# Optimization experiments

Hardware: AMD Instinct MI355X
Metric: run time of the kernel (lower is better)

Reference implementation:

```python
import jax, jax.numpy as jnp
import numpy as np

H, DH = 16, 64  # heads, dim_head (inner_dim = 1024)
VARIANCE_CONSTANT = 1.0


def setup_inputs() -> dict:
    key = jax.random.key(0)
    ks = jax.random.split(key, 6)
    b, n, m, dim = 8, 4096, 64, 1024
    inner = H * DH
    x = jax.random.normal(ks[0], (b, n, dim), dtype=jnp.float32)
    latents = jax.random.normal(ks[1], (b, m, dim), dtype=jnp.float32)
    mask = jax.random.randint(ks[2], (b, n), 0, 2).astype(bool)  # True = masked out
    sd = 1.0 / np.sqrt(dim)
    Wq = jax.random.normal(ks[3], (inner, dim), dtype=jnp.float32) * sd
    Wkv = jax.random.normal(ks[4], (2 * inner, dim), dtype=jnp.float32) * sd
    Wout = jax.random.normal(ks[5], (dim, inner), dtype=jnp.float32) * sd
    return {"x": x, "latents": latents, "mask": mask, "Wq": Wq, "Wkv": Wkv, "Wout": Wout}


def _split_heads(t):  # b n (h d) -> b h n d
    b, n, _ = t.shape
    return t.reshape(b, n, H, DH).transpose(0, 2, 1, 3)


def reference(x, latents, mask, Wq, Wkv, Wout):
    b, n, dim = x.shape
    scale = DH ** -0.5
    q = latents @ Wq.T                      # b m inner
    k, v = jnp.split(x @ Wkv.T, 2, axis=-1)  # b n inner each
    q = _split_heads(q) * scale             # b h m d
    k = _split_heads(k)                     # b h n d
    v = _split_heads(v)
    sim = jnp.einsum('bhid,bhjd->bhij', q, k)  # b h m n
    max_neg = -jnp.finfo(sim.dtype).max
    sim = jnp.where(mask[:, None, None, :], max_neg, sim)
    sim_new = sim - jax.lax.stop_gradient(sim.max(axis=-1, keepdims=True))
    # cross-query (dim=-2) unbiased variance -> std over latents, shape b h n
    std = jnp.sqrt(jnp.var(sim_new, axis=-2, ddof=1) + 1e-4)
    std = jnp.where(mask[:, None, :], VARIANCE_CONSTANT, std)
    loss_variance = jnp.mean(jax.nn.relu(VARIANCE_CONSTANT - std))
    attn = jax.nn.softmax(sim_new, axis=-1)
    out = jnp.einsum('bhij,bhjd->bhid', attn, v)         # b h m d
    out = out.transpose(0, 2, 1, 3).reshape(b, -1, H * DH)  # b m inner
    out = out @ Wout.T                                    # b m dim
    return out, loss_variance
```

## Files before the change

### kernel.cpp

```cpp
#include <hip/hip_runtime.h>


using u16 = unsigned short;
typedef short bf16x8_t __attribute__((ext_vector_type(8)));
typedef float f32x4_t __attribute__((ext_vector_type(4)));

__device__ __forceinline__ u16 f2bf(float f) {
    union { float f; unsigned u; } v; v.f = f;
    unsigned r = v.u + 0x7fffu + ((v.u >> 16) & 1u);
    return (u16)(r >> 16);
}

template <typename T> __device__ __forceinline__ T cvt_out(float v);
template <> __device__ __forceinline__ float cvt_out<float>(float v) { return v; }
template <> __device__ __forceinline__ u16   cvt_out<u16>(float v)   { return f2bf(v); }

__device__ __forceinline__ void cp16(const void* g, void* l) {
    __builtin_amdgcn_global_load_lds((const __attribute__((address_space(1))) unsigned int*)g,
                                     (__attribute__((address_space(3))) unsigned int*)l, 16, 0, 0);
}

__global__ void cvt_all(const float* __restrict__ x, const float* __restrict__ lat,
                        const float* __restrict__ wq, const float* __restrict__ wkv,
                        const float* __restrict__ wout,
                        u16* __restrict__ xb, u16* __restrict__ latb,
                        u16* __restrict__ wqb, u16* __restrict__ wkvb,
                        u16* __restrict__ woutb) {
    int i = blockIdx.x * 256 + threadIdx.x;
    const float* s; u16* d; int off; float sc = 1.f;
    if (i < 8388608)      { s = x;    d = xb;    off = i; }
    else if (i < 8519680) { s = lat;  d = latb;  off = i - 8388608; }
    else if (i < 8781824) { s = wq;   d = wqb;   off = i - 8519680; sc = 0.125f; }
    else if (i < 9306112) { s = wkv;  d = wkvb;  off = i - 8781824; }
    else if (i < 9568256) { s = wout; d = woutb; off = i - 9306112; }
    else return;
    float4 v = ((const float4*)s)[off];
    ushort4 o;
    o.x = f2bf(v.x * sc); o.y = f2bf(v.y * sc);
    o.z = f2bf(v.z * sc); o.w = f2bf(v.w * sc);
    ((ushort4*)d)[off] = o;
}


__device__ __forceinline__ void stage_half(const u16* __restrict__ G, u16* L,
                                           int grow0, int kt, int tid) {
    const int row8 = tid >> 3;
    const int pcb = tid & 7;
    const int sc = (pcb ^ (row8 & 7)) * 8;
    const int k0 = kt * 64;
    const int wu = (tid >> 6) * 512;
#pragma unroll
    for (int r = 0; r < 2; ++r)
        cp16(G + (size_t)(grow0 + r * 64 + row8) * 1024 + k0 + sc, L + r * 4096 + wu);
}

template <bool E12, bool E34, int WAIT>
__device__ __forceinline__ void tile_phases(
    const u16* At, const u16* Bt,
    const u16* __restrict__ gA, u16* lA, int rowA, int ktA,
    const u16* __restrict__ gB, u16* lB, int rowB, int ktB,
    int wm, int wn, int frow, int pc0, int pc1, int tid,
    f32x4_t (&acc)[8][4]) {
    bf16x8_t aF[4][2], bF[4][2];
#pragma unroll
    for (int i = 0; i < 4; ++i) {
        const u16* p = At + (wm * 128 + i * 16 + frow) * 64;
        aF[i][0] = *(const bf16x8_t*)(p + pc0);
        aF[i][1] = *(const bf16x8_t*)(p + pc1);
    }
#pragma unroll
    for (int j = 0; j < 4; ++j)
        bF[j][0] = *(const bf16x8_t*)(Bt + (wn * 64 + j * 16 + frow) * 64 + pc0);
    if (E12) stage_half(gA, lA, rowA, ktA, tid);
    __builtin_amdgcn_s_barrier();
    asm volatile("s_waitcnt lgkmcnt(0)" ::: "memory");
    __builtin_amdgcn_s_setprio(1);
#pragma unroll
    for (int i = 0; i < 4; ++i)
#pragma unroll
        for (int j = 0; j < 4; ++j)
            acc[i][j] = __builtin_amdgcn_mfma_f32_16x16x32_bf16(aF[i][0], bF[j][0], acc[i][j], 0, 0, 0);
    __builtin_amdgcn_s_setprio(0);
    __builtin_amdgcn_s_barrier();
#pragma unroll
    for (int j = 0; j < 4; ++j)
        bF[j][1] = *(const bf16x8_t*)(Bt + (wn * 64 + j * 16 + frow) * 64 + pc1);
    if (E12) stage_half(gA, lA + 8192, rowA + 128, ktA, tid);
    __builtin_amdgcn_s_barrier();
    asm volatile("s_waitcnt lgkmcnt(0)" ::: "memory");
    __builtin_amdgcn_s_setprio(1);
#pragma unroll
    for (int i = 0; i < 4; ++i)
#pragma unroll
        for (int j = 0; j < 4; ++j)
            acc[i][j] = __builtin_amdgcn_mfma_f32_16x16x32_bf16(aF[i][1], bF[j][1], acc[i][j], 0, 0, 0);
    __builtin_amdgcn_s_setprio(0);
    __builtin_amdgcn_s_barrier();
#pragma unroll
    for (int i = 0; i < 4; ++i) {
        const u16* p = At + (wm * 128 + (i + 4) * 16 + frow) * 64;
        aF[i][0] = *(const bf16x8_t*)(p + pc0);
        aF[i][1] = *(const bf16x8_t*)(p + pc1);
    }
    if (E34) stage_half(gB, lB, rowB, ktB, tid);
    __builtin_amdgcn_s_barrier();
    asm volatile("s_waitcnt lgkmcnt(0)" ::: "memory");
    __builtin_amdgcn_s_setprio(1);
#pragma unroll
    for (int i = 0; i < 4; ++i)
#pragma unroll
        for (int j = 0; j < 4; ++j)
            acc[i + 4][j] = __builtin_amdgcn_mfma_f32_16x16x32_bf16(aF[i][0], bF[j][0], acc[i + 4][j], 0, 0, 0);
    __builtin_amdgcn_s_setprio(0);
    __builtin_amdgcn_s_barrier();
    if (E34) stage_half(gB, lB + 8192, rowB + 128, ktB, tid);
    if (WAIT == 4)      asm volatile("s_waitcnt vmcnt(4)" ::: "memory");
    else if (WAIT == 0) asm volatile("s_waitcnt vmcnt(0)" ::: "memory");
    __builtin_amdgcn_s_barrier();
    __builtin_amdgcn_s_setprio(1);
#pragma unroll
    for (int i = 0; i < 4; ++i)
#pragma unroll
        for (int j = 0; j < 4; ++j)
            acc[i + 4][j] = __builtin_amdgcn_mfma_f32_16x16x32_bf16(aF[i][1], bF[j][1], acc[i + 4][j], 0, 0, 0);
    __builtin_amdgcn_s_setprio(0);
    __builtin_amdgcn_s_barrier();
}

__global__ __launch_bounds__(512, 2) void gemm_kv8(const u16* __restrict__ A,
                                                   const u16* __restrict__ B,
                                                   const u16* __restrict__ Qb,
                                                   const int* __restrict__ mask,
                                                   u16* __restrict__ Kc,
                                                   u16* __restrict__ Vt,
                                                   float* __restrict__ Mg2) {
    __shared__ __align__(16) u16 smem[65536];
    u16* A0 = smem;
    u16* A1 = smem + 16384;
    u16* B0 = smem + 32768;
    u16* B1 = smem + 49152;
    const int tid = threadIdx.x;
    const int wid = tid >> 6, lane = tid & 63;
    const int wm = wid >> 2, wn = wid & 3;
    const int frow = lane & 15, fq = lane >> 4;
    const int pc0 = (fq ^ (frow & 7)) * 8;
    const int pc1 = ((4 + fq) ^ (frow & 7)) * 8;
    const int fid = blockIdx.x;
    const int xcd = fid & 7, l = fid >> 3;
    const int by = xcd * 16 + (l >> 3), bx = l & 7;
    const int bm = by * 256, bn = bx * 256;

    f32x4_t acc[8][4];
#pragma unroll
    for (int i = 0; i < 8; ++i)
#pragma unroll
        for (int j = 0; j < 4; ++j) acc[i][j] = (f32x4_t){0.f, 0.f, 0.f, 0.f};

    stage_half(B, B0, bn, 0, tid);        stage_half(B, B0 + 8192, bn + 128, 0, tid);
    stage_half(A, A0, bm, 0, tid);        stage_half(A, A0 + 8192, bm + 128, 0, tid);
    stage_half(B, B1, bn, 1, tid);        stage_half(B, B1 + 8192, bn + 128, 1, tid);
    asm volatile("s_waitcnt vmcnt(4)" ::: "memory");
    __builtin_amdgcn_s_barrier();

    for (int t = 0; t < 7; ++t) {
        tile_phases<true, true, 4>(A0, B0, A, A1, bm, 2 * t + 1, B, B0, bn, 2 * t + 2,
                                   wm, wn, frow, pc0, pc1, tid, acc);
        tile_phases<true, true, 4>(A1, B1, A, A0, bm, 2 * t + 2, B, B1, bn, 2 * t + 3,
                                   wm, wn, frow, pc0, pc1, tid, acc);
    }
    tile_phases<true, false, 0>(A0, B0, A, A1, bm, 15, B, B1, bn, 0,
                                wm, wn, frow, pc0, pc1, tid, acc);
    tile_phases<false, false, -1>(A1, B1, A, A0, bm, 0, B, B1, bn, 0,
                                  wm, wn, frow, pc0, pc1, tid, acc);

    if (bx < 4) {
        const int bb = bm >> 12, jb = bm & 4095, chunk = by & 15;
        u16* Kl = smem;
#pragma unroll
        for (int i = 0; i < 8; ++i)
#pragma unroll
            for (int j = 0; j < 4; ++j) {
                const int cc0 = wn * 64 + j * 16 + frow;
#pragma unroll
                for (int r = 0; r < 4; ++r) {
                    const int jr = wm * 128 + i * 16 + fq * 4 + r;
                    Kl[jr * 256 + (((cc0 >> 3) ^ (jr & 7)) * 8) + (cc0 & 7)] = f2bf(acc[i][j][r]);
                }
            }
        __syncthreads();
#pragma unroll
        for (int p = 0; p < 16; ++p) {
            const int idx = p * 512 + tid;
            const int jr = idx >> 5, cb = idx & 31;
            bf16x8_t v = *(const bf16x8_t*)(Kl + jr * 256 + ((cb ^ (jr & 7)) * 8));
            *(bf16x8_t*)(Kc + (size_t)(bm + jr) * 1024 + bn + cb * 8) = v;
        }
        const int hh = wid >> 1, jn = (wid & 1) * 128;
        const int hc = (bx << 2) + hh;
        int mk[8];
#pragma unroll
        for (int jf = 0; jf < 8; ++jf)
            mk[jf] = mask[bb * 4096 + jb + jn + jf * 16 + frow];
        f32x4_t s2[4][8];
#pragma unroll
        for (int i = 0; i < 4; ++i)
#pragma unroll
            for (int jf = 0; jf < 8; ++jf) s2[i][jf] = (f32x4_t){0.f, 0.f, 0.f, 0.f};
#pragma unroll
        for (int ks = 0; ks < 2; ++ks) {
            bf16x8_t aq[4], bk[8];
#pragma unroll
            for (int i = 0; i < 4; ++i)
                aq[i] = *(const bf16x8_t*)(Qb + (size_t)(bb * 64 + i * 16 + frow) * 1024 +
                                           hc * 64 + ks * 32 + fq * 8);
#pragma unroll
            for (int jf = 0; jf < 8; ++jf) {
                const int jr = jn + jf * 16 + frow;
                bk[jf] = *(const bf16x8_t*)(Kl + jr * 256 +
                                            (((hh * 8 + ks * 4 + fq) ^ (jr & 7)) * 8));
            }
#pragma unroll
            for (int i = 0; i < 4; ++i)
#pragma unroll
                for (int jf = 0; jf < 8; ++jf)
                    s2[i][jf] = __builtin_amdgcn_mfma_f32_16x16x32_bf16(aq[i], bk[jf], s2[i][jf], 0, 0, 0);
        }
        float ml[16];
#pragma unroll
        for (int i = 0; i < 16; ++i) ml[i] = -3.0e38f;
#pragma unroll
        for (int jf = 0; jf < 8; ++jf)
            if (!mk[jf])
#pragma unroll
                for (int i = 0; i < 4; ++i)
#pragma unroll
                    for (int r = 0; r < 4; ++r)
                        ml[i * 4 + r] = fmaxf(ml[i * 4 + r], s2[i][jf][r]);
#pragma unroll
        for (int i = 0; i < 16; ++i) {
            float v = ml[i];
            v = fmaxf(v, __shfl_xor(v, 1)); v = fmaxf(v, __shfl_xor(v, 2));
            v = fmaxf(v, __shfl_xor(v, 4)); v = fmaxf(v, __shfl_xor(v, 8));
            ml[i] = v;
        }
        __syncthreads();
        float* Mp = (float*)smem;
        if ((lane & 15) == 0)
#pragma unroll
            for (int i = 0; i < 4; ++i)
#pragma unroll
                for (int r = 0; r < 4; ++r)
                    Mp[wid * 64 + i * 16 + fq * 4 + r] = ml[i * 4 + r];
        __syncthreads();
        if (tid < 256) {
            const int h2 = tid >> 6, m = tid & 63;
            Mg2[((size_t)(bb * 16 + (bx << 2) + h2) * 16 + chunk) * 64 + m] =
                fmaxf(Mp[(2 * h2) * 64 + m], Mp[(2 * h2 + 1) * 64 + m]);
        }
        return;
    }

    const int vb0 = bn - 1024;
    const int b = bm >> 12, jb = bm & 4095;
    u16* Ct = smem;
#pragma unroll
    for (int ph = 0; ph < 2; ++ph) {
        __syncthreads();
        if ((wn >> 1) == ph) {
#pragma unroll
            for (int i = 0; i < 8; ++i)
#pragma unroll
                for (int j = 0; j < 4; ++j) {
                    const int vdl = (wn & 1) * 64 + j * 16 + frow;
                    const int jl = wm * 128 + i * 16 + fq * 4;
                    ushort4 pk;
                    pk.x = f2bf(acc[i][j][0]); pk.y = f2bf(acc[i][j][1]);
                    pk.z = f2bf(acc[i][j][2]); pk.w = f2bf(acc[i][j][3]);
                    *(ushort4*)(Ct + vdl * 264 + jl) = pk;
                }
        }
        __syncthreads();
#pragma unroll
        for (int p = 0; p < 8; ++p) {
            const int idx = p * 512 + tid;
            const int vdl = idx >> 5;
            const int jl = (idx & 31) * 8;
            bf16x8_t v = *(const bf16x8_t*)(Ct + vdl * 264 + jl);
            const int vd = vb0 + ph * 128 + vdl;
            const size_t addr = ((size_t)(b * 16 + (vd >> 6)) * 64 + (vd & 63)) * 4096 + jb + jl;
            *(bf16x8_t*)(Vt + addr) = v;
        }
    }
}

template <typename OutT>
__global__ __launch_bounds__(256) void gemm_bt64(const u16* __restrict__ A,
                                                 const u16* __restrict__ B,
                                                 OutT* __restrict__ C,
                                                 int M, int N, int K) {
    __shared__ __align__(16) u16 As[64 * 64];
    __shared__ __align__(16) u16 Bs[64 * 64];
    const int tid = threadIdx.x;
    const int wid = tid >> 6, lane = tid & 63;
    const int bm = blockIdx.y * 64, bn = blockIdx.x * 64;
    const int srow = lane >> 3;
    const int scol = ((lane & 7) ^ srow) * 8;
    const int frow = lane & 15;
    const int wr = (wid >> 1) * 32, wc = (wid & 1) * 32;

    f32x4_t acc[2][2];
#pragma unroll
    for (int i = 0; i < 2; ++i)
#pragma unroll
        for (int j = 0; j < 2; ++j) acc[i][j] = (f32x4_t){0.f, 0.f, 0.f, 0.f};

    for (int k0 = 0; k0 < K; k0 += 64) {
#pragma unroll
        for (int t = 0; t < 2; ++t) {
            const int c = wid * 2 + t;
            const int r = c * 8 + srow;
            cp16(A + (size_t)(bm + r) * K + k0 + scol, As + c * 512);
            cp16(B + (size_t)(bn + r) * K + k0 + scol, Bs + c * 512);
        }
        __syncthreads();
#pragma unroll
        for (int ks = 0; ks < 2; ++ks) {
            const int grp = (((ks * 4 + (lane >> 4)) ^ (frow & 7)) * 8);
            bf16x8_t af[2], bfv[2];
#pragma unroll
            for (int i = 0; i < 2; ++i) {
                af[i]  = *(const bf16x8_t*)(As + (wr + i * 16 + frow) * 64 + grp);
                bfv[i] = *(const bf16x8_t*)(Bs + (wc + i * 16 + frow) * 64 + grp);
            }
#pragma unroll
            for (int i = 0; i < 2; ++i)
#pragma unroll
                for (int j = 0; j < 2; ++j)
                    acc[i][j] = __builtin_amdgcn_mfma_f32_16x16x32_bf16(af[i], bfv[j], acc[i][j], 0, 0, 0);
        }
        __syncthreads();
    }
    const int cr = (lane >> 4) * 4, cc = lane & 15;
#pragma unroll
    for (int i = 0; i < 2; ++i)
#pragma unroll
        for (int j = 0; j < 2; ++j) {
            size_t base = (size_t)(bm + wr + i * 16 + cr) * N + (bn + wc + j * 16 + cc);
#pragma unroll
            for (int r = 0; r < 4; ++r)
                C[base + (size_t)r * N] = cvt_out<OutT>(acc[i][j][r]);
        }
}

__global__ __launch_bounds__(256, 2) void attn_pv(const u16* __restrict__ q,
                                                  const u16* __restrict__ kbuf,
                                                  const u16* __restrict__ vtbuf,
                                                  const int* __restrict__ mask,
                                                  const float* __restrict__ Mg,
                                                  float* __restrict__ Opart,
                                                  float* __restrict__ Rpart,
                                                  float* __restrict__ loss) {
    const int c = blockIdx.x & 3, bh = blockIdx.x >> 2, b = bh >> 4, h = bh & 15;
    const int tid = threadIdx.x, wid = tid >> 6, lane = tid & 63;
    const int frow = lane & 15, cr = (lane >> 4) * 4;
    const int srow = lane >> 3, scol = ((lane & 7) ^ srow) * 8;

    __shared__ __align__(16) u16 qs[64 * 64];
    __shared__ __align__(16) u16 wbuf[4][2][4096];
    __shared__ float Mrow[64];
    __shared__ float RpS[4][64];
    __shared__ float lossP[4];

    const size_t kbase  = (size_t)b * 4096 * 1024 + (size_t)h * 64;
    const size_t vtbase = (size_t)bh * 64 * 4096;
    const int cb = c * 1024;
    u16* Kw = &wbuf[wid][0][0];
    u16* Vw = &wbuf[wid][1][0];

#pragma unroll
    for (int t = 0; t < 2; ++t) {
        int cq = wid * 2 + t;
        int r = cq * 8 + srow;
        cp16(q + (size_t)(b * 64 + r) * 1024 + h * 64 + scol, qs + cq * 512);
    }
    if (tid < 64) {
        float m = -3.0e38f;
#pragma unroll
        for (int cc = 0; cc < 16; ++cc) m = fmaxf(m, Mg[(size_t)(bh * 16 + cc) * 64 + tid]);
        Mrow[tid] = m;
    }
    __syncthreads();

    f32x4_t oacc[4][4];
#pragma unroll
    for (int i = 0; i < 4; ++i)
#pragma unroll
        for (int j = 0; j < 4; ++j) oacc[i][j] = (f32x4_t){0.f, 0.f, 0.f, 0.f};
    float rloc[16];
#pragma unroll
    for (int i = 0; i < 16; ++i) rloc[i] = 0.f;
    float lossacc = 0.f;

    for (int sc = 0; sc < 4; ++sc) {
        const int j0 = cb + (sc * 4 + wid) * 64;
#pragma unroll
        for (int t = 0; t < 8; ++t) {
            int r = t * 8 + srow;
            cp16(kbuf + kbase + (size_t)(j0 + r) * 1024 + scol, Kw + t * 512);
        }
#pragma unroll
        for (int t = 0; t < 8; ++t) {
            int d = t * 8 + srow;
            cp16(vtbuf + vtbase + (size_t)d * 4096 + j0 + scol, Vw + t * 512);
        }
        __builtin_amdgcn_s_waitcnt(0);

        f32x4_t sacc[4][4];
#pragma unroll
        for (int i = 0; i < 4; ++i)
#pragma unroll
            for (int j = 0; j < 4; ++j) sacc[i][j] = (f32x4_t){0.f, 0.f, 0.f, 0.f};
#pragma unroll
        for (int ks2 = 0; ks2 < 2; ++ks2) {
            const int grp = (((ks2 * 4 + (lane >> 4)) ^ (frow & 7)) * 8);
            bf16x8_t af[4], bfv[4];
#pragma unroll
            for (int i = 0; i < 4; ++i) {
                af[i]  = *(const bf16x8_t*)(qs + (i * 16 + frow) * 64 + grp);
                bfv[i] = *(const bf16x8_t*)(Kw + (i * 16 + frow) * 64 + grp);
            }
#pragma unroll
            for (int i = 0; i < 4; ++i)
#pragma unroll
                for (int j = 0; j < 4; ++j)
                    sacc[i][j] = __builtin_amdgcn_mfma_f32_16x16x32_bf16(af[i], bfv[j], sacc[i][j], 0, 0, 0);
        }

#pragma unroll
        for (int nt = 0; nt < 4; ++nt) {
            const int jl = nt * 16 + frow;
            const bool msk = mask[b * 4096 + j0 + jl] != 0;
            const int jh = jl >> 3, jlo = jl & 7;
            float c1 = 0.f, c2 = 0.f;
#pragma unroll
            for (int mt = 0; mt < 4; ++mt) {
#pragma unroll
                for (int r = 0; r < 4; ++r) {
                    const int row = mt * 16 + cr + r;
                    const float t = sacc[mt][nt][r] - Mrow[row];
                    const float p = msk ? 0.f : __expf(t);
                    rloc[mt * 4 + r] += p;
                    c1 += msk ? 0.f : t;
                    c2 += msk ? 0.f : t * t;
                    Kw[row * 64 + ((jh ^ (row & 7)) * 8) + jlo] = f2bf(p);
                }
            }
            c1 += __shfl_xor(c1, 16); c1 += __shfl_xor(c1, 32);
            c2 += __shfl_xor(c2, 16); c2 += __shfl_xor(c2, 32);
            if (lane < 16 && !msk) {
                const float var = (c2 - c1 * c1 * (1.f / 64.f)) * (1.f / 63.f);
                lossacc += fmaxf(1.f - sqrtf(var + 1e-4f), 0.f);
            }
        }
#pragma unroll
        for (int ks2 = 0; ks2 < 2; ++ks2) {
            const int grp = (((ks2 * 4 + (lane >> 4)) ^ (frow & 7)) * 8);
            bf16x8_t pa[4], vb[4];
#pragma unroll
            for (int i = 0; i < 4; ++i) {
                pa[i] = *(const bf16x8_t*)(Kw + (i * 16 + frow) * 64 + grp);
                vb[i] = *(const bf16x8_t*)(Vw + (i * 16 + frow) * 64 + grp);
            }
#pragma unroll
            for (int i = 0; i < 4; ++i)
#pragma unroll
                for (int j = 0; j < 4; ++j)
                    oacc[i][j] = __builtin_amdgcn_mfma_f32_16x16x32_bf16(pa[i], vb[j], oacc[i][j], 0, 0, 0);
        }
    }

    float* Osw = (float*)(&wbuf[0][0][0]) + wid * 4096;
#pragma unroll
    for (int i = 0; i < 4; ++i)
#pragma unroll
        for (int j = 0; j < 4; ++j)
#pragma unroll
            for (int r = 0; r < 4; ++r)
                Osw[(i * 16 + cr + r) * 64 + j * 16 + frow] = oacc[i][j][r];

#pragma unroll
    for (int i = 0; i < 16; ++i) {
        float v = rloc[i];
        v += __shfl_xor(v, 1); v += __shfl_xor(v, 2);
        v += __shfl_xor(v, 4); v += __shfl_xor(v, 8);
        rloc[i] = v;
    }
    if ((lane & 15) == 0) {
#pragma unroll
        for (int mt = 0; mt < 4; ++mt)
#pragma unroll
            for (int r = 0; r < 4; ++r)
                RpS[wid][mt * 16 + cr + r] = rloc[mt * 4 + r];
    }
    float v = lossacc;
    v += __shfl_xor(v, 1); v += __shfl_xor(v, 2); v += __shfl_xor(v, 4);
    v += __shfl_xor(v, 8); v += __shfl_xor(v, 16); v += __shfl_xor(v, 32);
    if (lane == 0) lossP[wid] = v;
    __syncthreads();

    const float4* Ob4 = (const float4*)(&wbuf[0][0][0]);
    const size_t ob = (size_t)(bh * 4 + c) * 4096;
#pragma unroll
    for (int p = 0; p < 4; ++p) {
        const int e = tid + p * 256;
        float4 s0 = Ob4[e];
        float4 s1 = Ob4[e + 1024];
        float4 s2 = Ob4[e + 2048];
        float4 s3 = Ob4[e + 3072];
        float4 o;
        o.x = s0.x + s1.x + s2.x + s3.x;
        o.y = s0.y + s1.y + s2.y + s3.y;
        o.z = s0.z + s1.z + s2.z + s3.z;
        o.w = s0.w + s1.w + s2.w + s3.w;
        ((float4*)(Opart + ob))[e] = o;
    }
    if (tid < 64)
        Rpart[(size_t)(bh * 4 + c) * 64 + tid] =
            RpS[0][tid] + RpS[1][tid] + RpS[2][tid] + RpS[3][tid];
    if (tid == 0)
        atomicAdd(loss, (lossP[0] + lossP[1] + lossP[2] + lossP[3]) * (1.f / 524288.f));
}

__global__ __launch_bounds__(256) void attn_fin(const float* __restrict__ Opart,
                                                const float* __restrict__ Rpart,
                                                u16* __restrict__ ao) {
    const int bh = blockIdx.x, b = bh >> 4, h = bh & 15;
    const int tid = threadIdx.x;
    __shared__ float Rt[64];
    if (tid < 64) {
        float r = 0.f;
#pragma unroll
        for (int cc = 0; cc < 4; ++cc) r += Rpart[(size_t)(bh * 4 + cc) * 64 + tid];
        Rt[tid] = r;
    }
    __syncthreads();
    for (int e = tid; e < 4096; e += 256) {
        float o = 0.f;
#pragma unroll
        for (int cc = 0; cc < 4; ++cc) o += Opart[(size_t)(bh * 4 + cc) * 4096 + e];
        const int row = e >> 6, d = e & 63;
        ao[(size_t)(b * 64 + row) * 1024 + h * 64 + d] = f2bf(o / Rt[row]);
    }
}

extern "C" void kernel_launch(void* const* d_in, const int* in_sizes, int n_in,
                              void* d_out, int out_size, void* d_ws, size_t ws_size,
                              hipStream_t stream) {
    const float* x    = (const float*)d_in[0];
    const float* lat  = (const float*)d_in[1];
    const int*   mask = (const int*)d_in[2];
    const float* Wq   = (const float*)d_in[3];
    const float* Wkv  = (const float*)d_in[4];
    const float* Wout = (const float*)d_in[5];
    float* out = (float*)d_out;

    char* ws = (char*)d_ws;
    u16* x_bf    = (u16*)(ws);
    u16* kbuf    = (u16*)(ws + 67108864);
    u16* vtbuf   = (u16*)(ws + 134217728);
    u16* wq_bf   = (u16*)(ws + 201326592);
    u16* wkv_bf  = (u16*)(ws + 203423744);
    u16* wout_bf = (u16*)(ws + 207618048);
    u16* lat_bf  = (u16*)(ws + 209715200);
    u16* q_bf    = (u16*)(ws + 210763776);
    u16* ao_bf   = (u16*)(ws + 211812352);
    float* Mg    = (float*)(ws + 201326592);
    float* Opart = (float*)(ws + 1048576);
    float* Rpart = (float*)(ws + 1048576 + 8388608);

    hipMemsetAsync(out + 524288, 0, 4, stream);

    cvt_all<<<37376, 256, 0, stream>>>(x, lat, Wq, Wkv, Wout,
                                       x_bf, lat_bf, wq_bf, wkv_bf, wout_bf);

    dim3 blk(256);
    gemm_bt64<u16><<<dim3(16, 8), blk, 0, stream>>>(lat_bf, wq_bf, q_bf, 512, 1024, 1024);
    gemm_kv8<<<dim3(1024), dim3(512), 0, stream>>>(x_bf, wkv_bf, q_bf, mask, kbuf, vtbuf, Mg);
    attn_pv<<<512, blk, 0, stream>>>(q_bf, kbuf, vtbuf, mask, Mg, Opart, Rpart, out + 524288);
    attn_fin<<<128, blk, 0, stream>>>(Opart, Rpart, ao_bf);
    gemm_bt64<float><<<dim3(16, 8), blk, 0, stream>>>(ao_bf, wout_bf, out, 512, 1024, 1024);
}
```

Measured before the change: 435.4 us.

## Split attn_pv waves by query rows with shared double-buffered K/V tiles

Reworks attn_pv so each wave owns 16 query rows across all keys instead of 64 rows over its own key slice. K/V tiles are shared by the block and double-buffered, with global-to-LDS prefetch of the next tile overlapping compute. Cross-query variance sums are reduced through LDS per tile, and the final cross-wave O reduction is dropped. Lower LDS and register use allows raising launch bounds to 3 blocks, at the cost of two to three block barriers per tile.

```diff
diff --git a/kernel.cpp b/kernel.cpp
--- a/kernel.cpp
+++ b/kernel.cpp
@@ -352,7 +352,7 @@
         }
 }
 
-__global__ __launch_bounds__(256, 2) void attn_pv(const u16* __restrict__ q,
+__global__ __launch_bounds__(256, 3) void attn_pv(const u16* __restrict__ q,
                                                   const u16* __restrict__ kbuf,
                                                   const u16* __restrict__ vtbuf,
                                                   const int* __restrict__ mask,
@@ -362,26 +362,26 @@
                                                   float* __restrict__ loss) {
     const int c = blockIdx.x & 3, bh = blockIdx.x >> 2, b = bh >> 4, h = bh & 15;
     const int tid = threadIdx.x, wid = tid >> 6, lane = tid & 63;
-    const int frow = lane & 15, cr = (lane >> 4) * 4;
-    const int srow = lane >> 3, scol = ((lane & 7) ^ srow) * 8;
-
-    __shared__ __align__(16) u16 qs[64 * 64];
-    __shared__ __align__(16) u16 wbuf[4][2][4096];
+    const int frow = lane & 15, fq = lane >> 4;
+    const int srow = lane >> 3, scol8 = ((lane & 7) ^ srow) * 8;
+
+    __shared__ __align__(16) u16 qs[4096];
+    __shared__ __align__(16) u16 kv[4][4096];
+    __shared__ __align__(16) u16 Pw[4][1024];
+    __shared__ float cstat[4][2][64];
     __shared__ float Mrow[64];
-    __shared__ float RpS[4][64];
-    __shared__ float lossP[4];
 
     const size_t kbase  = (size_t)b * 4096 * 1024 + (size_t)h * 64;
     const size_t vtbase = (size_t)bh * 64 * 4096;
     const int cb = c * 1024;
-    u16* Kw = &wbuf[wid][0][0];
-    u16* Vw = &wbuf[wid][1][0];
+    const int s_c = tid & 7, s_r0 = tid >> 3;
+    const int wu = wid * 512;
 
 #pragma unroll
     for (int t = 0; t < 2; ++t) {
         int cq = wid * 2 + t;
         int r = cq * 8 + srow;
-        cp16(q + (size_t)(b * 64 + r) * 1024 + h * 64 + scol, qs + cq * 512);
+        cp16(q + (size_t)(b * 64 + r) * 1024 + h * 64 + scol8, qs + cq * 512);
     }
     if (tid < 64) {
         float m = -3.0e38f;
@@ -389,146 +389,159 @@
         for (int cc = 0; cc < 16; ++cc) m = fmaxf(m, Mg[(size_t)(bh * 16 + cc) * 64 + tid]);
         Mrow[tid] = m;
     }
-    __syncthreads();
-
-    f32x4_t oacc[4][4];
-#pragma unroll
-    for (int i = 0; i < 4; ++i)
-#pragma unroll
-        for (int j = 0; j < 4; ++j) oacc[i][j] = (f32x4_t){0.f, 0.f, 0.f, 0.f};
-    float rloc[16];
-#pragma unroll
-    for (int i = 0; i < 16; ++i) rloc[i] = 0.f;
+#pragma unroll
+    for (int sel = 0; sel < 2; ++sel) {
+        const int j0 = cb + sel * 64;
+#pragma unroll
+        for (int rnd = 0; rnd < 2; ++rnd) {
+            const int row = rnd * 32 + s_r0;
+            const int sc = (s_c ^ (row & 7)) * 8;
+            cp16(kbuf + kbase + (size_t)(j0 + row) * 1024 + sc, kv[sel] + rnd * 2048 + wu);
+        }
+#pragma unroll
+        for (int rnd = 0; rnd < 2; ++rnd) {
+            const int row = rnd * 32 + s_r0;
+            const int sc = (s_c ^ (row & 7)) * 8;
+            cp16(vtbuf + vtbase + (size_t)row * 4096 + j0 + sc, kv[2 + sel] + rnd * 2048 + wu);
+        }
+    }
+    asm volatile("s_waitcnt vmcnt(4) lgkmcnt(0)" ::: "memory");
+    __builtin_amdgcn_s_barrier();
+
+    bf16x8_t af[2];
+#pragma unroll
+    for (int ks = 0; ks < 2; ++ks)
+        af[ks] = *(const bf16x8_t*)(qs + (wid * 16 + frow) * 64 + (((ks * 4 + fq) ^ (frow & 7)) * 8));
+    float mr[4];
+#pragma unroll
+    for (int r = 0; r < 4; ++r) mr[r] = Mrow[wid * 16 + fq * 4 + r];
+
+    f32x4_t oacc[4];
+#pragma unroll
+    for (int dj = 0; dj < 4; ++dj) oacc[dj] = (f32x4_t){0.f, 0.f, 0.f, 0.f};
+    float rloc[4] = {0.f, 0.f, 0.f, 0.f};
     float lossacc = 0.f;
 
-    for (int sc = 0; sc < 4; ++sc) {
-        const int j0 = cb + (sc * 4 + wid) * 64;
-#pragma unroll
-        for (int t = 0; t < 8; ++t) {
-            int r = t * 8 + srow;
-            cp16(kbuf + kbase + (size_t)(j0 + r) * 1024 + scol, Kw + t * 512);
-        }
-#pragma unroll
-        for (int t = 0; t < 8; ++t) {
-            int d = t * 8 + srow;
-            cp16(vtbuf + vtbase + (size_t)d * 4096 + j0 + scol, Vw + t * 512);
-        }
-        __builtin_amdgcn_s_waitcnt(0);
-
-        f32x4_t sacc[4][4];
-#pragma unroll
-        for (int i = 0; i < 4; ++i)
-#pragma unroll
-            for (int j = 0; j < 4; ++j) sacc[i][j] = (f32x4_t){0.f, 0.f, 0.f, 0.f};
-#pragma unroll
-        for (int ks2 = 0; ks2 < 2; ++ks2) {
-            const int grp = (((ks2 * 4 + (lane >> 4)) ^ (frow & 7)) * 8);
-            bf16x8_t af[4], bfv[4];
-#pragma unroll
-            for (int i = 0; i < 4; ++i) {
-                af[i]  = *(const bf16x8_t*)(qs + (i * 16 + frow) * 64 + grp);
-                bfv[i] = *(const bf16x8_t*)(Kw + (i * 16 + frow) * 64 + grp);
-            }
-#pragma unroll
-            for (int i = 0; i < 4; ++i)
-#pragma unroll
-                for (int j = 0; j < 4; ++j)
-                    sacc[i][j] = __builtin_amdgcn_mfma_f32_16x16x32_bf16(af[i], bfv[j], sacc[i][j], 0, 0, 0);
-        }
-
-#pragma unroll
-        for (int nt = 0; nt < 4; ++nt) {
-            const int jl = nt * 16 + frow;
-            const bool msk = mask[b * 4096 + j0 + jl] != 0;
-            const int jh = jl >> 3, jlo = jl & 7;
-            float c1 = 0.f, c2 = 0.f;
-#pragma unroll
-            for (int mt = 0; mt < 4; ++mt) {
-#pragma unroll
-                for (int r = 0; r < 4; ++r) {
-                    const int row = mt * 16 + cr + r;
-                    const float t = sacc[mt][nt][r] - Mrow[row];
-                    const float p = msk ? 0.f : __expf(t);
-                    rloc[mt * 4 + r] += p;
-                    c1 += msk ? 0.f : t;
-                    c2 += msk ? 0.f : t * t;
-                    Kw[row * 64 + ((jh ^ (row & 7)) * 8) + jlo] = f2bf(p);
-                }
-            }
-            c1 += __shfl_xor(c1, 16); c1 += __shfl_xor(c1, 32);
-            c2 += __shfl_xor(c2, 16); c2 += __shfl_xor(c2, 32);
-            if (lane < 16 && !msk) {
-                const float var = (c2 - c1 * c1 * (1.f / 64.f)) * (1.f / 63.f);
+    for (int t = 0; t < 16; ++t) {
+        const int sel = t & 1;
+        const int j0 = cb + t * 64;
+        const u16* Kc_ = kv[sel];
+        const u16* Vc_ = kv[2 + sel];
+        int mk[4];
+#pragma unroll
+        for (int j = 0; j < 4; ++j) mk[j] = mask[b * 4096 + j0 + j * 16 + frow];
+
+        f32x4_t sacc[4];
+#pragma unroll
+        for (int j = 0; j < 4; ++j) sacc[j] = (f32x4_t){0.f, 0.f, 0.f, 0.f};
+#pragma unroll
+        for (int ks = 0; ks < 2; ++ks) {
+            const int kswz = ((ks * 4 + fq) ^ (frow & 7)) * 8;
+#pragma unroll
+            for (int j = 0; j < 4; ++j) {
+                bf16x8_t bk = *(const bf16x8_t*)(Kc_ + (j * 16 + frow) * 64 + kswz);
+                sacc[j] = __builtin_amdgcn_mfma_f32_16x16x32_bf16(af[ks], bk, sacc[j], 0, 0, 0);
+            }
+        }
+        float c1l[4] = {0.f, 0.f, 0.f, 0.f}, c2l[4] = {0.f, 0.f, 0.f, 0.f};
+#pragma unroll
+        for (int j = 0; j < 4; ++j) {
+#pragma unroll
+            for (int r = 0; r < 4; ++r) {
+                const int rowl = fq * 4 + r;
+                const float tv = sacc[j][r] - mr[r];
+                const float p = mk[j] ? 0.f : __expf(tv);
+                rloc[r] += p;
+                c1l[j] += mk[j] ? 0.f : tv;
+                c2l[j] += mk[j] ? 0.f : tv * tv;
+                const int jc = j * 2 + (frow >> 3);
+                Pw[wid][rowl * 64 + ((jc ^ (rowl & 7)) * 8) + (frow & 7)] = f2bf(p);
+            }
+            c1l[j] += __shfl_xor(c1l[j], 16); c1l[j] += __shfl_xor(c1l[j], 32);
+            c2l[j] += __shfl_xor(c2l[j], 16); c2l[j] += __shfl_xor(c2l[j], 32);
+            if (fq == 0) {
+                cstat[wid][0][j * 16 + frow] = c1l[j];
+                cstat[wid][1][j * 16 + frow] = c2l[j];
+            }
+        }
+        asm volatile("s_waitcnt lgkmcnt(0)" ::: "memory");
+        __builtin_amdgcn_s_barrier();
+        if (wid == 0) {
+            const float c1t = cstat[0][0][lane] + cstat[1][0][lane] + cstat[2][0][lane] + cstat[3][0][lane];
+            const float c2t = cstat[0][1][lane] + cstat[1][1][lane] + cstat[2][1][lane] + cstat[3][1][lane];
+            if (!mask[b * 4096 + j0 + lane]) {
+                const float var = (c2t - c1t * c1t * (1.f / 64.f)) * (1.f / 63.f);
                 lossacc += fmaxf(1.f - sqrtf(var + 1e-4f), 0.f);
             }
         }
 #pragma unroll
-        for (int ks2 = 0; ks2 < 2; ++ks2) {
-            const int grp = (((ks2 * 4 + (lane >> 4)) ^ (frow & 7)) * 8);
-            bf16x8_t pa[4], vb[4];
-#pragma unroll
-            for (int i = 0; i < 4; ++i) {
-                pa[i] = *(const bf16x8_t*)(Kw + (i * 16 + frow) * 64 + grp);
-                vb[i] = *(const bf16x8_t*)(Vw + (i * 16 + frow) * 64 + grp);
-            }
-#pragma unroll
-            for (int i = 0; i < 4; ++i)
-#pragma unroll
-                for (int j = 0; j < 4; ++j)
-                    oacc[i][j] = __builtin_amdgcn_mfma_f32_16x16x32_bf16(pa[i], vb[j], oacc[i][j], 0, 0, 0);
-        }
-    }
-
-    float* Osw = (float*)(&wbuf[0][0][0]) + wid * 4096;
-#pragma unroll
-    for (int i = 0; i < 4; ++i)
-#pragma unroll
-        for (int j = 0; j < 4; ++j)
-#pragma unroll
-            for (int r = 0; r < 4; ++r)
-                Osw[(i * 16 + cr + r) * 64 + j * 16 + frow] = oacc[i][j][r];
-
-#pragma unroll
-    for (int i = 0; i < 16; ++i) {
-        float v = rloc[i];
+        for (int ks = 0; ks < 2; ++ks) {
+            const int kswz = ((ks * 4 + fq) ^ (frow & 7)) * 8;
+            bf16x8_t pa = *(const bf16x8_t*)(Pw[wid] + frow * 64 + kswz);
+#pragma unroll
+            for (int dj = 0; dj < 4; ++dj) {
+                bf16x8_t vb = *(const bf16x8_t*)(Vc_ + (dj * 16 + frow) * 64 + kswz);
+                oacc[dj] = __builtin_amdgcn_mfma_f32_16x16x32_bf16(pa, vb, oacc[dj], 0, 0, 0);
+            }
+        }
+        asm volatile("s_waitcnt lgkmcnt(0)" ::: "memory");
+        __builtin_amdgcn_s_barrier();
+        if (t < 14) {
+            const int jn = cb + (t + 2) * 64;
+#pragma unroll
+            for (int rnd = 0; rnd < 2; ++rnd) {
+                const int row = rnd * 32 + s_r0;
+                const int sc = (s_c ^ (row & 7)) * 8;
+                cp16(kbuf + kbase + (size_t)(jn + row) * 1024 + sc, kv[sel] + rnd * 2048 + wu);
+            }
+#pragma unroll
+            for (int rnd = 0; rnd < 2; ++rnd) {
+                const int row = rnd * 32 + s_r0;
+                const int sc = (s_c ^ (row & 7)) * 8;
+                cp16(vtbuf + vtbase + (size_t)row * 4096 + jn + sc, kv[2 + sel] + rnd * 2048 + wu);
+            }
+            asm volatile("s_waitcnt vmcnt(4)" ::: "memory");
+            __builtin_amdgcn_s_barrier();
+        } else if (t == 14) {
+            asm volatile("s_waitcnt vmcnt(0)" ::: "memory");
+            __builtin_amdgcn_s_barrier();
+        }
+    }
+
+    float* Ol = (float*)&kv[0][0];
+#pragma unroll
+    for (int dj = 0; dj < 4; ++dj)
+#pragma unroll
+        for (int r = 0; r < 4; ++r)
+            Ol[(wid * 16 + fq * 4 + r) * 64 + dj * 16 + frow] = oacc[dj][r];
+
+#pragma unroll
+    for (int r = 0; r < 4; ++r) {
+        float v = rloc[r];
         v += __shfl_xor(v, 1); v += __shfl_xor(v, 2);
         v += __shfl_xor(v, 4); v += __shfl_xor(v, 8);
-        rloc[i] = v;
-    }
-    if ((lane & 15) == 0) {
-#pragma unroll
-        for (int mt = 0; mt < 4; ++mt)
-#pragma unroll
-            for (int r = 0; r < 4; ++r)
-                RpS[wid][mt * 16 + cr + r] = rloc[mt * 4 + r];
-    }
-    float v = lossacc;
-    v += __shfl_xor(v, 1); v += __shfl_xor(v, 2); v += __shfl_xor(v, 4);
-    v += __shfl_xor(v, 8); v += __shfl_xor(v, 16); v += __shfl_xor(v, 32);
-    if (lane == 0) lossP[wid] = v;
-    __syncthreads();
-
-    const float4* Ob4 = (const float4*)(&wbuf[0][0][0]);
+        rloc[r] = v;
+    }
+    if (frow == 0)
+#pragma unroll
+        for (int r = 0; r < 4; ++r)
+            Rpart[(size_t)(bh * 4 + c) * 64 + wid * 16 + fq * 4 + r] = rloc[r];
+
+    if (wid == 0) {
+        float v = lossacc;
+        v += __shfl_xor(v, 1); v += __shfl_xor(v, 2); v += __shfl_xor(v, 4);
+        v += __shfl_xor(v, 8); v += __shfl_xor(v, 16); v += __shfl_xor(v, 32);
+        if (lane == 0) atomicAdd(loss, v * (1.f / 524288.f));
+    }
+
+    asm volatile("s_waitcnt lgkmcnt(0)" ::: "memory");
+    __builtin_amdgcn_s_barrier();
     const size_t ob = (size_t)(bh * 4 + c) * 4096;
 #pragma unroll
     for (int p = 0; p < 4; ++p) {
-        const int e = tid + p * 256;
-        float4 s0 = Ob4[e];
-        float4 s1 = Ob4[e + 1024];
-        float4 s2 = Ob4[e + 2048];
-        float4 s3 = Ob4[e + 3072];
-        float4 o;
-        o.x = s0.x + s1.x + s2.x + s3.x;
-        o.y = s0.y + s1.y + s2.y + s3.y;
-        o.z = s0.z + s1.z + s2.z + s3.z;
-        o.w = s0.w + s1.w + s2.w + s3.w;
-        ((float4*)(Opart + ob))[e] = o;
-    }
-    if (tid < 64)
-        Rpart[(size_t)(bh * 4 + c) * 64 + tid] =
-            RpS[0][tid] + RpS[1][tid] + RpS[2][tid] + RpS[3][tid];
-    if (tid == 0)
-        atomicAdd(loss, (lossP[0] + lossP[1] + lossP[2] + lossP[3]) * (1.f / 524288.f));
+        const int e = p * 256 + tid;
+        ((float4*)(Opart + ob))[e] = ((const float4*)Ol)[e];
+    }
 }
 
 __global__ __launch_bounds__(256) void attn_fin(const float* __restrict__ Opart,
```

New measurement: 422.1 us. -3.1%, faster.
